# Kernel tuning notes

Hardware: AMD Instinct MI355X
Metric: run time of the kernel (lower is better)

The kernel has to match this reference:

```python
import jax, jax.numpy as jnp
import numpy as np

# --- config (matches init_kwargs) ---
H = 16          # num_attention_heads
DH = 64         # size_per_head
U = H * DH      # units = 1024
M = 8           # num_memory_slots
L = M + 1       # memory slots + current input row
R = 2 * M + 1   # relative position range
EPS = 1e-6
FORGET_BIAS = 1.0
INPUT_BIAS = 0.0
SCALE = 1.0 / np.sqrt(DH)


def _rel_emb():
    # sinusoidal relative-position embedding table [2M+1, U]
    p = np.arange(-M, M + 1, dtype=np.float64)
    i = np.arange(U)
    expo = np.where(i % 2 == 0, i, i - 1) / U
    ang = p[:, None] / np.power(10000.0, expo)[None, :]
    tab = np.where(i % 2 == 0, np.sin(ang), np.cos(ang))
    return jnp.asarray(tab, dtype=jnp.float32)

REL_EMB = _rel_emb()
# rel index table: idx[q,k] = q - k + M  (replaces one-hot pos_table matmul)
_qi = jnp.arange(L)
REL_IDX = _qi[:, None] - _qi[None, :] + M  # [L, L]


def _hard_sigmoid(x):
    return jnp.clip(0.2 * x + 0.5, 0.0, 1.0)


def _ln(x, g, b):
    m = jnp.mean(x, axis=-1, keepdims=True)
    v = jnp.var(x, axis=-1, keepdims=True)
    return (x - m) * jax.lax.rsqrt(v + EPS) * g + b


def setup_inputs() -> dict:
    key = jax.random.key(0)
    ks = jax.random.split(key, 12)
    B, T, DIN = 32, 128, 1024
    s = 0.02
    return {
        "x": jax.random.normal(ks[0], (B, T, DIN), jnp.float32),
        "input_kernel": jax.random.normal(ks[1], (DIN, U), jnp.float32) * s,
        "input_bias": jnp.zeros((U,), jnp.float32),
        "gate_kernel": jax.random.normal(ks[2], (DIN, 2 * U), jnp.float32) * s,
        "recurrent_kernel": jax.random.normal(ks[3], (U, 2 * U), jnp.float32) * s,
        "recurrent_bias": jnp.zeros((2 * U,), jnp.float32),
        "attention_kernel": jax.random.normal(ks[4], (U, 3 * U), jnp.float32) * s,
        "attention_bias": jnp.zeros((3 * U,), jnp.float32),
        "mlp_kernel": jax.random.normal(ks[5], (U, 2 * U), jnp.float32) * s,
        "mlp_bias": jnp.zeros((2 * U,), jnp.float32),
        "ln_gamma": jnp.ones((2 * U,), jnp.float32),
        "ln_beta": jnp.zeros((2 * U,), jnp.float32),
        "rel_kernel": jax.random.normal(ks[6], (U, U), jnp.float32) * s,
    }


def _forward(x, input_kernel, input_bias, gate_kernel, recurrent_kernel,
             recurrent_bias, attention_kernel, attention_bias, mlp_kernel,
             mlp_bias, ln_gamma, ln_beta, rel_kernel):
    B = x.shape[0]
    # relative key projection, shared across steps: [R, H, DH]
    r = (REL_EMB @ rel_kernel).reshape(R, H, DH)

    def step(mem, xt):
        # xt: [B, DIN]; mem: [B, M, U]
        xp = xt @ input_kernel + input_bias              # [B, U]
        mp = jnp.concatenate([mem, xp[:, None, :]], axis=1)  # [B, L, U]
        qkv = mp @ attention_kernel + attention_bias     # [B, L, 3U]
        q, k, v = jnp.split(qkv, 3, axis=-1)
        q = q.reshape(B, L, H, DH).transpose(0, 2, 1, 3)  # [B,H,L,DH]
        k = k.reshape(B, L, H, DH).transpose(0, 2, 1, 3)
        v = v.reshape(B, L, H, DH).transpose(0, 2, 1, 3)
        scores = jnp.einsum('bhqd,bhkd->bhqk', q, k) * SCALE
        rsc = jnp.einsum('bhqd,rhd->bhqr', q, r) * SCALE  # [B,H,L,R]
        scores = scores + rsc[:, :, jnp.arange(L)[:, None], REL_IDX]
        p = jax.nn.softmax(scores, axis=-1)
        attn = jnp.einsum('bhqk,bhkd->bhqd', p, v)
        attn = attn.transpose(0, 2, 1, 3).reshape(B, L, U)
        a1 = _ln(mp + attn, ln_gamma[:U], ln_beta[:U])
        h = jax.nn.gelu(a1 @ mlp_kernel[:, :U] + mlp_bias[:U])
        m2 = h @ mlp_kernel[:, U:] + mlp_bias[U:]
        cand = _ln(a1 + m2, ln_gamma[U:], ln_beta[U:])
        # LSTM-style per-slot gating
        g = (xt @ gate_kernel)[:, None, :] + mp @ recurrent_kernel + recurrent_bias
        ig, fg = jnp.split(g, 2, axis=-1)
        ig = _hard_sigmoid(ig + INPUT_BIAS)
        fg = _hard_sigmoid(fg + FORGET_BIAS)
        nmp = fg * mp + ig * jnp.tanh(cand)              # [B, L, U]
        return nmp[:, :M, :], nmp[:, -1, :]

    mem0 = jnp.zeros((B, M, U), x.dtype)
    _, ys = jax.lax.scan(step, mem0, x.transpose(1, 0, 2))
    return ys.transpose(1, 0, 2)  # [B, T, U]


def reference(x, input_kernel, input_bias, gate_kernel, recurrent_kernel,
              recurrent_bias, attention_kernel, attention_bias, mlp_kernel,
              mlp_bias, ln_gamma, ln_beta, rel_kernel):
    return _forward(x, input_kernel, input_bias, gate_kernel, recurrent_kernel,
                    recurrent_bias, attention_kernel, attention_bias,
                    mlp_kernel, mlp_bias, ln_gamma, ln_beta, rel_kernel)
```

## Files before the change

### kernel.cpp

```cpp
#include <hip/hip_runtime.h>
#include <hip/hip_bf16.h>
#include <math.h>

#define BB 32
#define TT 128
#define UU 1024
#define MM 8
#define LL 9
#define RR 17
#define MROWS 288
#define NKS 4
#define KLEN 256

typedef __bf16 bf16x8 __attribute__((ext_vector_type(8)));
typedef float f32x4 __attribute__((ext_vector_type(4)));
typedef float f32x8 __attribute__((ext_vector_type(8)));

__device__ __forceinline__ void split3(float v, __bf16* x1, __bf16* x2, __bf16* x3)
{
    __bf16 h1 = (__bf16)v;  float r = v - (float)h1;
    __bf16 h2 = (__bf16)r;  r -= (float)h2;
    *x1 = h1; *x2 = h2; *x3 = (__bf16)r;
}

__device__ __forceinline__ void split8(const f32x8 v, bf16x8& a, bf16x8& b, bf16x8& c)
{
#pragma unroll
    for (int j = 0; j < 8; ++j) {
        float f = v[j];
        __bf16 h1 = (__bf16)f; float r = f - (float)h1;
        __bf16 h2 = (__bf16)r; r -= (float)h2;
        a[j] = h1; b[j] = h2; c[j] = (__bf16)r;
    }
}

__device__ __forceinline__ float gelu_f(float x)
{
    float t = tanhf(0.7978845608028654f * (x + 0.044715f * x * x * x));
    return 0.5f * x * (1.f + t);
}

template<int CG>
__global__ __launch_bounds__(256) void gemmks(
    const float* __restrict__ A,
    const __bf16* __restrict__ B1, const __bf16* __restrict__ B2,
    const __bf16* __restrict__ B3,
    float* __restrict__ P, int N, int GdivP)
{
    int tid = threadIdx.x, wave = tid >> 6, lane = tid & 63;
    int bid = blockIdx.x;
    int x = bid & 7, inner = bid >> 3;
    int q = inner % GdivP, rowT = inner / GdivP;
    int g = x + 8 * q;
    int colT = g / NKS, ks = g % NKS;

    int lr = lane & 15, kg = lane >> 4;
    int row0 = rowT * 32 + (wave & 1) * 16;
    int col0 = colT * (CG * 32) + (wave >> 1) * (CG * 16);
    int kbase = ks * KLEN;

    const float* Ap = A + (size_t)(row0 + lr) * 1024 + kbase + kg * 8;
    size_t boff = (size_t)(col0 + lr) * 1024 + kbase + kg * 8;

    f32x4 acc[CG];
#pragma unroll
    for (int c = 0; c < CG; ++c) acc[c] = (f32x4){0.f, 0.f, 0.f, 0.f};

#pragma unroll
    for (int k = 0; k < KLEN; k += 32) {
        f32x8 af = *(const f32x8*)(Ap + k);
        bf16x8 a1, a2, a3;
        split8(af, a1, a2, a3);
#pragma unroll
        for (int c = 0; c < CG; ++c) {
            size_t o = boff + (size_t)c * 16 * 1024 + k;
            bf16x8 b1 = *(const bf16x8*)(B1 + o);
            bf16x8 b2 = *(const bf16x8*)(B2 + o);
            bf16x8 b3 = *(const bf16x8*)(B3 + o);
            acc[c] = __builtin_amdgcn_mfma_f32_16x16x32_bf16(a1, b1, acc[c], 0, 0, 0);
            acc[c] = __builtin_amdgcn_mfma_f32_16x16x32_bf16(a1, b2, acc[c], 0, 0, 0);
            acc[c] = __builtin_amdgcn_mfma_f32_16x16x32_bf16(a2, b1, acc[c], 0, 0, 0);
            acc[c] = __builtin_amdgcn_mfma_f32_16x16x32_bf16(a1, b3, acc[c], 0, 0, 0);
            acc[c] = __builtin_amdgcn_mfma_f32_16x16x32_bf16(a2, b2, acc[c], 0, 0, 0);
            acc[c] = __builtin_amdgcn_mfma_f32_16x16x32_bf16(a3, b1, acc[c], 0, 0, 0);
        }
    }

    int r0 = row0 + kg * 4;
    float* Pk = P + (size_t)ks * MROWS * N;
#pragma unroll
    for (int c = 0; c < CG; ++c) {
        int col = col0 + c * 16 + lr;
#pragma unroll
        for (int r = 0; r < 4; ++r)
            Pk[(size_t)(r0 + r) * N + col] = acc[c][r];
    }
}

__global__ __launch_bounds__(256) void add4(
    const float* __restrict__ P, const float* __restrict__ bias,
    float* __restrict__ out, int N, int act, int total4)
{
    int idx = blockIdx.x * 256 + threadIdx.x;
    if (idx >= total4) return;
    size_t e = (size_t)idx * 4;
    size_t SP = (size_t)MROWS * N;
    int col = (int)(e % N);
    f32x4 p0 = *(const f32x4*)(P + e);
    f32x4 p1 = *(const f32x4*)(P + SP + e);
    f32x4 p2 = *(const f32x4*)(P + 2 * SP + e);
    f32x4 p3 = *(const f32x4*)(P + 3 * SP + e);
    f32x4 bv = *(const f32x4*)(bias + col);
    f32x4 s;
#pragma unroll
    for (int j = 0; j < 4; ++j) {
        float v = ((p0[j] + p1[j]) + (p2[j] + p3[j])) + bv[j];
        s[j] = act ? gelu_f(v) : v;
    }
    *(f32x4*)(out + e) = s;
}

template<int CG>
__device__ __forceinline__ void tile6(
    const float* __restrict__ A,
    const __bf16* __restrict__ B1, const __bf16* __restrict__ B2,
    const __bf16* __restrict__ B3,
    const float* __restrict__ bias, float* __restrict__ C,
    int ldc, int act, int row0, int col0, int lane)
{
    int lr = lane & 15, kofs = (lane >> 4) * 8;
    const float* Ap = A + (size_t)(row0 + lr) * 1024 + kofs;
    size_t boff = (size_t)(col0 + lr) * 1024 + kofs;
    f32x4 acc[CG];
#pragma unroll
    for (int c = 0; c < CG; ++c) acc[c] = (f32x4){0.f, 0.f, 0.f, 0.f};

    for (int k = 0; k < 1024; k += 32) {
        f32x8 af = *(const f32x8*)(Ap + k);
        bf16x8 a1, a2, a3;
        split8(af, a1, a2, a3);
#pragma unroll
        for (int c = 0; c < CG; ++c) {
            size_t o = boff + (size_t)c * 16 * 1024 + k;
            bf16x8 b1 = *(const bf16x8*)(B1 + o);
            bf16x8 b2 = *(const bf16x8*)(B2 + o);
            bf16x8 b3 = *(const bf16x8*)(B3 + o);
            acc[c] = __builtin_amdgcn_mfma_f32_16x16x32_bf16(a1, b1, acc[c], 0, 0, 0);
            acc[c] = __builtin_amdgcn_mfma_f32_16x16x32_bf16(a1, b2, acc[c], 0, 0, 0);
            acc[c] = __builtin_amdgcn_mfma_f32_16x16x32_bf16(a2, b1, acc[c], 0, 0, 0);
            acc[c] = __builtin_amdgcn_mfma_f32_16x16x32_bf16(a1, b3, acc[c], 0, 0, 0);
            acc[c] = __builtin_amdgcn_mfma_f32_16x16x32_bf16(a2, b2, acc[c], 0, 0, 0);
            acc[c] = __builtin_amdgcn_mfma_f32_16x16x32_bf16(a3, b1, acc[c], 0, 0, 0);
        }
    }

    int r0 = row0 + (lane >> 4) * 4;
#pragma unroll
    for (int c = 0; c < CG; ++c) {
        int col = col0 + c * 16 + lr;
        float bv = bias ? bias[col] : 0.f;
#pragma unroll
        for (int r = 0; r < 4; ++r) {
            float v = acc[c][r] + bv;
            if (act == 1) v = gelu_f(v);
            C[(size_t)(r0 + r) * ldc + col] = v;
        }
    }
}

__global__ __launch_bounds__(256) void gemm6(
    const float* __restrict__ A,
    const __bf16* __restrict__ B1, const __bf16* __restrict__ B2,
    const __bf16* __restrict__ B3,
    const float* __restrict__ bias, float* __restrict__ C, int ldc, int act)
{
    int wave = threadIdx.x >> 6, lane = threadIdx.x & 63;
    int row0 = blockIdx.y * 32 + (wave >> 1) * 16;
    int col0 = blockIdx.x * 128 + (wave & 1) * 64;
    tile6<4>(A, B1, B2, B3, bias, C, ldc, act, row0, col0, lane);
}

__global__ __launch_bounds__(256) void transpose_split(
    const float* __restrict__ in,
    __bf16* __restrict__ o1, __bf16* __restrict__ o2, __bf16* __restrict__ o3,
    int N)
{
    __shared__ float t[32][33];
    int tx = threadIdx.x & 31, ty = threadIdx.x >> 5;
    int k0 = blockIdx.y * 32, n0 = blockIdx.x * 32;
#pragma unroll
    for (int i = 0; i < 4; ++i)
        t[ty + i * 8][tx] = in[(size_t)(k0 + ty + i * 8) * N + n0 + tx];
    __syncthreads();
#pragma unroll
    for (int i = 0; i < 4; ++i) {
        float v = t[tx][ty + i * 8];
        size_t off = (size_t)(n0 + ty + i * 8) * 1024 + k0 + tx;
        split3(v, o1 + off, o2 + off, o3 + off);
    }
}

#define BKK 16
__global__ __launch_bounds__(256) void gemm_f32(
    const float* __restrict__ A, const float* __restrict__ B,
    float* __restrict__ C, int M, int N, int K)
{
    __shared__ float As[BKK][65];
    __shared__ float Bs[BKK][64];
    int tid = threadIdx.x;
    int row0 = blockIdx.y * 64, col0 = blockIdx.x * 64;
    int ty = tid >> 4, tx = tid & 15;
    float acc[4][4];
#pragma unroll
    for (int i = 0; i < 4; ++i)
#pragma unroll
        for (int j = 0; j < 4; ++j) acc[i][j] = 0.f;
    for (int k0 = 0; k0 < K; k0 += BKK) {
        {
            int r = tid >> 2, kv = (tid & 3) * 4;
            float4 v = make_float4(0.f, 0.f, 0.f, 0.f);
            int gr = row0 + r;
            if (gr < M) v = *(const float4*)(A + (size_t)gr * K + k0 + kv);
            As[kv + 0][r] = v.x; As[kv + 1][r] = v.y;
            As[kv + 2][r] = v.z; As[kv + 3][r] = v.w;
        }
        {
            int r = tid >> 4, cv = (tid & 15) * 4;
            float4 v = *(const float4*)(B + (size_t)(k0 + r) * N + col0 + cv);
            *(float4*)&Bs[r][cv] = v;
        }
        __syncthreads();
#pragma unroll
        for (int kk = 0; kk < BKK; ++kk) {
            float a[4], b[4];
#pragma unroll
            for (int j = 0; j < 4; ++j) a[j] = As[kk][ty * 4 + j];
#pragma unroll
            for (int j = 0; j < 4; ++j) b[j] = Bs[kk][tx * 4 + j];
#pragma unroll
            for (int i = 0; i < 4; ++i)
#pragma unroll
                for (int j = 0; j < 4; ++j) acc[i][j] += a[i] * b[j];
        }
        __syncthreads();
    }
#pragma unroll
    for (int i = 0; i < 4; ++i) {
        int gr = row0 + ty * 4 + i;
        if (gr >= M) continue;
#pragma unroll
        for (int j = 0; j < 4; ++j)
            C[(size_t)gr * N + col0 + tx * 4 + j] = acc[i][j];
    }
}

__global__ void relemb_kernel(float* __restrict__ tab)
{
    int p = blockIdx.x;
    float pv = (float)(p - MM);
    for (int i = threadIdx.x; i < UU; i += blockDim.x) {
        float expo = (float)(i & ~1) * (1.0f / (float)UU);
        float scale = exp2f(-expo * 13.287712379549449f);
        float ang = pv * scale;
        tab[p * UU + i] = (i & 1) ? cosf(ang) : sinf(ang);
    }
}

__global__ void init_mp(const float* __restrict__ xp_all, float* __restrict__ mp)
{
    int row = blockIdx.x;
    int b = row / LL, l = row % LL;
    for (int u = threadIdx.x; u < UU; u += blockDim.x)
        mp[(size_t)row * UU + u] = (l == MM) ? xp_all[((size_t)b * TT) * UU + u] : 0.f;
}

__global__ __launch_bounds__(512) void attn_ln(
    const float* __restrict__ qkvg, const float* __restrict__ rproj,
    const float* __restrict__ mp,
    const float* __restrict__ gamma, const float* __restrict__ beta,
    float* __restrict__ a1)
{
    __shared__ float sA[LL][UU];
    __shared__ float red[16];
    int b = blockIdx.x;
    int tid = threadIdx.x;
    int wave = tid >> 6, lane = tid & 63;

    for (int hh = 0; hh < 2; ++hh) {
        int h = wave + hh * 8;
        const float* base = qkvg + (size_t)b * LL * 5120 + h * 64 + lane;
        float q[LL], k[LL], v[LL], r[RR];
#pragma unroll
        for (int l = 0; l < LL; ++l) {
            q[l] = base[l * 5120];
            k[l] = base[l * 5120 + 1024];
            v[l] = base[l * 5120 + 2048];
        }
#pragma unroll
        for (int rp = 0; rp < RR; ++rp) r[rp] = rproj[rp * UU + h * 64 + lane];
#pragma unroll
        for (int qr = 0; qr < LL; ++qr) {
            float sc[LL];
#pragma unroll
            for (int kr = 0; kr < LL; ++kr) {
                float prod = q[qr] * (k[kr] + r[qr - kr + MM]);
#pragma unroll
                for (int o = 32; o > 0; o >>= 1) prod += __shfl_xor(prod, o);
                sc[kr] = prod * 0.125f;
            }
            float m = sc[0];
#pragma unroll
            for (int kr = 1; kr < LL; ++kr) m = fmaxf(m, sc[kr]);
            float s = 0.f;
#pragma unroll
            for (int kr = 0; kr < LL; ++kr) { sc[kr] = expf(sc[kr] - m); s += sc[kr]; }
            float inv = 1.0f / s;
            float acc = 0.f;
#pragma unroll
            for (int kr = 0; kr < LL; ++kr) acc += sc[kr] * v[kr];
            sA[qr][h * 64 + lane] = acc * inv;
        }
    }
    __syncthreads();

    for (int l = 0; l < LL; ++l) {
        size_t row = (size_t)(b * LL + l);
        float x0 = mp[row * UU + tid] + sA[l][tid];
        float x1 = mp[row * UU + tid + 512] + sA[l][tid + 512];
        float s = x0 + x1, ss = x0 * x0 + x1 * x1;
#pragma unroll
        for (int o = 32; o > 0; o >>= 1) { s += __shfl_xor(s, o); ss += __shfl_xor(ss, o); }
        if (lane == 0) { red[wave * 2] = s; red[wave * 2 + 1] = ss; }
        __syncthreads();
        float S = 0.f, SS = 0.f;
#pragma unroll
        for (int w = 0; w < 8; ++w) { S += red[w * 2]; SS += red[w * 2 + 1]; }
        __syncthreads();
        float mean = S * (1.0f / UU);
        float var = SS * (1.0f / UU) - mean * mean;
        float rstd = rsqrtf(var + 1e-6f);
        a1[row * UU + tid]       = (x0 - mean) * rstd * gamma[tid] + beta[tid];
        a1[row * UU + tid + 512] = (x1 - mean) * rstd * gamma[tid + 512] + beta[tid + 512];
    }
}

__global__ __launch_bounds__(256) void finalize_step(
    const float* __restrict__ a1, const float* __restrict__ m2P,
    const float* __restrict__ bm,
    const float* __restrict__ qkvg, const float* __restrict__ gx_all,
    const float* __restrict__ xp_all,
    const float* __restrict__ gamma, const float* __restrict__ beta,
    float* __restrict__ mp, float* __restrict__ out, int t)
{
    __shared__ float red[8];
    int row = blockIdx.x;
    int b = row / LL, l = row % LL;
    int tid = threadIdx.x;
    int wave = tid >> 6, lane = tid & 63;
    const size_t SP = (size_t)MROWS * UU;

    float x[4];
    float s = 0.f, ss = 0.f;
#pragma unroll
    for (int j = 0; j < 4; ++j) {
        int u = tid + j * 256;
        size_t off = (size_t)row * UU + u;
        float m2v = ((m2P[off] + m2P[SP + off]) + (m2P[2 * SP + off] + m2P[3 * SP + off]))
                    + bm[1024 + u];
        x[j] = a1[off] + m2v;
        s += x[j]; ss += x[j] * x[j];
    }
#pragma unroll
    for (int o = 32; o > 0; o >>= 1) { s += __shfl_xor(s, o); ss += __shfl_xor(ss, o); }
    if (lane == 0) { red[wave * 2] = s; red[wave * 2 + 1] = ss; }
    __syncthreads();
    float S = 0.f, SS = 0.f;
#pragma unroll
    for (int w = 0; w < 4; ++w) { S += red[w * 2]; SS += red[w * 2 + 1]; }
    float mean = S * (1.0f / UU);
    float rstd = rsqrtf(SS * (1.0f / UU) - mean * mean + 1e-6f);

    size_t gxoff = ((size_t)b * TT + t) * 2048;
    size_t grow = (size_t)row * 5120 + 3072;
#pragma unroll
    for (int j = 0; j < 4; ++j) {
        int u = tid + j * 256;
        float cand = (x[j] - mean) * rstd * gamma[1024 + u] + beta[1024 + u];
        float tc = tanhf(cand);
        float gi = gx_all[gxoff + u]        + qkvg[grow + u];
        float gf = gx_all[gxoff + 1024 + u] + qkvg[grow + 1024 + u];
        float ig = fminf(fmaxf(0.2f * gi + 0.5f, 0.f), 1.f);
        float fg = fminf(fmaxf(0.2f * (gf + 1.0f) + 0.5f, 0.f), 1.f);
        size_t off = (size_t)row * UU + u;
        float nmp = fg * mp[off] + ig * tc;
        if (l < MM) {
            mp[off] = nmp;
        } else {
            out[((size_t)b * TT + t) * UU + u] = nmp;
            if (t + 1 < TT)
                mp[off] = xp_all[((size_t)b * TT + t + 1) * UU + u];
        }
    }
}

extern "C" void kernel_launch(void* const* d_in, const int* in_sizes, int n_in,
                              void* d_out, int out_size, void* d_ws, size_t ws_size,
                              hipStream_t stream)
{
    const float* x    = (const float*)d_in[0];
    const float* Wi   = (const float*)d_in[1];
    const float* bi   = (const float*)d_in[2];
    const float* Wg   = (const float*)d_in[3];
    const float* Wr   = (const float*)d_in[4];
    const float* br   = (const float*)d_in[5];
    const float* Wa   = (const float*)d_in[6];
    const float* ba   = (const float*)d_in[7];
    const float* Wm   = (const float*)d_in[8];
    const float* bm   = (const float*)d_in[9];
    const float* gam  = (const float*)d_in[10];
    const float* bet  = (const float*)d_in[11];
    const float* Wrel = (const float*)d_in[12];
    float* out = (float*)d_out;

    char* w = (char*)d_ws;
    float*  xp_all = (float*)w;  w += (size_t)BB*TT*UU*4;
    float*  gx_all = (float*)w;  w += (size_t)BB*TT*2048*4;
    size_t W1N = (size_t)5120 * 1024, WMN = (size_t)2048 * 1024;
    __bf16* W1a = (__bf16*)w;    w += W1N*2;
    __bf16* W1b = (__bf16*)w;    w += W1N*2;
    __bf16* W1c = (__bf16*)w;    w += W1N*2;
    __bf16* Wma = (__bf16*)w;    w += WMN*2;
    __bf16* Wmb = (__bf16*)w;    w += WMN*2;
    __bf16* Wmc = (__bf16*)w;    w += WMN*2;
    float*  b1    = (float*)w;   w += 5120*4;
    float*  tab   = (float*)w;   w += RR*UU*4;
    float*  rproj = (float*)w;   w += RR*UU*4;
    float*  mp    = (float*)w;   w += (size_t)MROWS*UU*4;
    float*  qkvg  = (float*)w;   w += (size_t)MROWS*5120*4;
    float*  a1    = (float*)w;   w += (size_t)MROWS*UU*4;
    float*  hbuf  = (float*)w;   w += (size_t)MROWS*UU*4;
    char* sbase = w;
    float*  qkvgP = (float*)w;   w += (size_t)NKS*MROWS*5120*4;
    float*  m1P   = (float*)w;   w += (size_t)NKS*MROWS*UU*4;
    float*  m2P   = (float*)w;   w += (size_t)NKS*MROWS*UU*4;
    __bf16* Wia = (__bf16*)sbase;
    __bf16* Wib = Wia + (size_t)1024 * 1024;
    __bf16* Wic = Wib + (size_t)1024 * 1024;
    __bf16* Wga = Wic + (size_t)1024 * 1024;
    __bf16* Wgb = Wga + (size_t)2048 * 1024;
    __bf16* Wgc = Wgb + (size_t)2048 * 1024;

    relemb_kernel<<<RR, 256, 0, stream>>>(tab);
    gemm_f32<<<dim3(UU / 64, 1), 256, 0, stream>>>(tab, Wrel, rproj, RR, UU, UU);
    transpose_split<<<dim3(3072 / 32, 32), 256, 0, stream>>>(Wa, W1a, W1b, W1c, 3072);
    transpose_split<<<dim3(2048 / 32, 32), 256, 0, stream>>>(
        Wr, W1a + (size_t)3072 * 1024, W1b + (size_t)3072 * 1024,
        W1c + (size_t)3072 * 1024, 2048);
    transpose_split<<<dim3(2048 / 32, 32), 256, 0, stream>>>(Wm, Wma, Wmb, Wmc, 2048);
    transpose_split<<<dim3(1024 / 32, 32), 256, 0, stream>>>(Wi, Wia, Wib, Wic, 1024);
    transpose_split<<<dim3(2048 / 32, 32), 256, 0, stream>>>(Wg, Wga, Wgb, Wgc, 2048);
    hipMemcpyAsync(b1, ba, 3072 * sizeof(float), hipMemcpyDeviceToDevice, stream);
    hipMemcpyAsync(b1 + 3072, br, 2048 * sizeof(float), hipMemcpyDeviceToDevice, stream);
    gemm6<<<dim3(UU / 128, (BB * TT) / 32), 256, 0, stream>>>(
        x, Wia, Wib, Wic, bi, xp_all, UU, 0);
    gemm6<<<dim3(2048 / 128, (BB * TT) / 32), 256, 0, stream>>>(
        x, Wga, Wgb, Wgc, nullptr, gx_all, 2048, 0);
    init_mp<<<MROWS, 256, 0, stream>>>(xp_all, mp);

    for (int t = 0; t < TT; ++t) {
        gemmks<2><<<2880, 256, 0, stream>>>(mp, W1a, W1b, W1c, qkvgP, 5120, 40);
        add4<<<(MROWS * 5120 / 4 + 255) / 256, 256, 0, stream>>>(
            qkvgP, b1, qkvg, 5120, 0, MROWS * 5120 / 4);
        attn_ln<<<BB, 512, 0, stream>>>(qkvg, rproj, mp, gam, bet, a1);
        gemmks<2><<<576, 256, 0, stream>>>(a1, Wma, Wmb, Wmc, m1P, UU, 8);
        add4<<<(MROWS * UU / 4 + 255) / 256, 256, 0, stream>>>(
            m1P, bm, hbuf, UU, 1, MROWS * UU / 4);
        gemmks<2><<<576, 256, 0, stream>>>(hbuf, Wma + (size_t)1024 * 1024,
                                           Wmb + (size_t)1024 * 1024,
                                           Wmc + (size_t)1024 * 1024, m2P, UU, 8);
        finalize_step<<<MROWS, 256, 0, stream>>>(a1, m2P, bm, qkvg, gx_all, xp_all,
                                                 gam, bet, mp, out, t);
    }
}
```

Baseline: 25.07 ms.

## Fold QKVG split-K reduction into consumers and prefetch B fragments in gemmks

The big per-step QKVG GEMM now uses 2 K-splits of 512 instead of 4 of 256, which halves the partial-sum traffic. The separate add4 reduction kernel is removed, and attn_ln and finalize_step sum the two partials plus bias directly. The gemmks inner loop also loads B fragments for two K-chunks ahead of the MFMAs to overlap loads with compute. In exchange there are fewer blocks for the QKVG GEMM (1440 instead of 2880), and each consumer does extra reads of the partial buffers.

```diff
diff --git a/kernel.cpp b/kernel.cpp
--- a/kernel.cpp
+++ b/kernel.cpp
@@ -9,8 +9,6 @@
 #define LL 9
 #define RR 17
 #define MROWS 288
-#define NKS 4
-#define KLEN 256
 
 typedef __bf16 bf16x8 __attribute__((ext_vector_type(8)));
 typedef float f32x4 __attribute__((ext_vector_type(4)));
@@ -40,7 +38,7 @@
     return 0.5f * x * (1.f + t);
 }
 
-template<int CG>
+template<int CG, int NKS, int KLEN>
 __global__ __launch_bounds__(256) void gemmks(
     const float* __restrict__ A,
     const __bf16* __restrict__ B1, const __bf16* __restrict__ B2,
@@ -66,8 +64,84 @@
 #pragma unroll
     for (int c = 0; c < CG; ++c) acc[c] = (f32x4){0.f, 0.f, 0.f, 0.f};
 
-#pragma unroll
-    for (int k = 0; k < KLEN; k += 32) {
+    for (int kc = 0; kc < KLEN; kc += 64) {
+        f32x8 af0 = *(const f32x8*)(Ap + kc);
+        f32x8 af1 = *(const f32x8*)(Ap + kc + 32);
+        bf16x8 bv[2][CG][3];
+#pragma unroll
+        for (int h = 0; h < 2; ++h)
+#pragma unroll
+            for (int c = 0; c < CG; ++c) {
+                size_t o = boff + (size_t)c * 16 * 1024 + kc + h * 32;
+                bv[h][c][0] = *(const bf16x8*)(B1 + o);
+                bv[h][c][1] = *(const bf16x8*)(B2 + o);
+                bv[h][c][2] = *(const bf16x8*)(B3 + o);
+            }
+#pragma unroll
+        for (int h = 0; h < 2; ++h) {
+            bf16x8 a1, a2, a3;
+            split8(h ? af1 : af0, a1, a2, a3);
+#pragma unroll
+            for (int c = 0; c < CG; ++c) {
+                bf16x8 b1 = bv[h][c][0], b2 = bv[h][c][1], b3 = bv[h][c][2];
+                acc[c] = __builtin_amdgcn_mfma_f32_16x16x32_bf16(a1, b1, acc[c], 0, 0, 0);
+                acc[c] = __builtin_amdgcn_mfma_f32_16x16x32_bf16(a1, b2, acc[c], 0, 0, 0);
+                acc[c] = __builtin_amdgcn_mfma_f32_16x16x32_bf16(a2, b1, acc[c], 0, 0, 0);
+                acc[c] = __builtin_amdgcn_mfma_f32_16x16x32_bf16(a1, b3, acc[c], 0, 0, 0);
+                acc[c] = __builtin_amdgcn_mfma_f32_16x16x32_bf16(a2, b2, acc[c], 0, 0, 0);
+                acc[c] = __builtin_amdgcn_mfma_f32_16x16x32_bf16(a3, b1, acc[c], 0, 0, 0);
+            }
+        }
+    }
+
+    int r0 = row0 + kg * 4;
+    float* Pk = P + (size_t)ks * MROWS * N;
+#pragma unroll
+    for (int c = 0; c < CG; ++c) {
+        int col = col0 + c * 16 + lr;
+#pragma unroll
+        for (int r = 0; r < 4; ++r)
+            Pk[(size_t)(r0 + r) * N + col] = acc[c][r];
+    }
+}
+
+__global__ __launch_bounds__(256) void add4gelu(
+    const float* __restrict__ P, const float* __restrict__ bias,
+    float* __restrict__ out, int N, int total4)
+{
+    int idx = blockIdx.x * 256 + threadIdx.x;
+    if (idx >= total4) return;
+    size_t e = (size_t)idx * 4;
+    size_t SP = (size_t)MROWS * N;
+    int col = (int)(e % N);
+    f32x4 p0 = *(const f32x4*)(P + e);
+    f32x4 p1 = *(const f32x4*)(P + SP + e);
+    f32x4 p2 = *(const f32x4*)(P + 2 * SP + e);
+    f32x4 p3 = *(const f32x4*)(P + 3 * SP + e);
+    f32x4 bv = *(const f32x4*)(bias + col);
+    f32x4 s;
+#pragma unroll
+    for (int j = 0; j < 4; ++j)
+        s[j] = gelu_f(((p0[j] + p1[j]) + (p2[j] + p3[j])) + bv[j]);
+    *(f32x4*)(out + e) = s;
+}
+
+template<int CG>
+__device__ __forceinline__ void tile6(
+    const float* __restrict__ A,
+    const __bf16* __restrict__ B1, const __bf16* __restrict__ B2,
+    const __bf16* __restrict__ B3,
+    const float* __restrict__ bias, float* __restrict__ C,
+    int ldc, int act, int row0, int col0, int lane)
+{
+    int lr = lane & 15, kofs = (lane >> 4) * 8;
+    const float* Ap = A + (size_t)(row0 + lr) * 1024 + kofs;
+    size_t boff = (size_t)(col0 + lr) * 1024 + kofs;
+    f32x4 acc[CG];
+#pragma unroll
+    for (int c = 0; c < CG; ++c) acc[c] = (f32x4){0.f, 0.f, 0.f, 0.f};
+
+    for (int k = 0; k < 1024; k += 32) {
         f32x8 af = *(const f32x8*)(Ap + k);
         bf16x8 a1, a2, a3;
         split8(af, a1, a2, a3);
@@ -86,74 +160,6 @@
         }
     }
 
-    int r0 = row0 + kg * 4;
-    float* Pk = P + (size_t)ks * MROWS * N;
-#pragma unroll
-    for (int c = 0; c < CG; ++c) {
-        int col = col0 + c * 16 + lr;
-#pragma unroll
-        for (int r = 0; r < 4; ++r)
-            Pk[(size_t)(r0 + r) * N + col] = acc[c][r];
-    }
-}
-
-__global__ __launch_bounds__(256) void add4(
-    const float* __restrict__ P, const float* __restrict__ bias,
-    float* __restrict__ out, int N, int act, int total4)
-{
-    int idx = blockIdx.x * 256 + threadIdx.x;
-    if (idx >= total4) return;
-    size_t e = (size_t)idx * 4;
-    size_t SP = (size_t)MROWS * N;
-    int col = (int)(e % N);
-    f32x4 p0 = *(const f32x4*)(P + e);
-    f32x4 p1 = *(const f32x4*)(P + SP + e);
-    f32x4 p2 = *(const f32x4*)(P + 2 * SP + e);
-    f32x4 p3 = *(const f32x4*)(P + 3 * SP + e);
-    f32x4 bv = *(const f32x4*)(bias + col);
-    f32x4 s;
-#pragma unroll
-    for (int j = 0; j < 4; ++j) {
-        float v = ((p0[j] + p1[j]) + (p2[j] + p3[j])) + bv[j];
-        s[j] = act ? gelu_f(v) : v;
-    }
-    *(f32x4*)(out + e) = s;
-}
-
-template<int CG>
-__device__ __forceinline__ void tile6(
-    const float* __restrict__ A,
-    const __bf16* __restrict__ B1, const __bf16* __restrict__ B2,
-    const __bf16* __restrict__ B3,
-    const float* __restrict__ bias, float* __restrict__ C,
-    int ldc, int act, int row0, int col0, int lane)
-{
-    int lr = lane & 15, kofs = (lane >> 4) * 8;
-    const float* Ap = A + (size_t)(row0 + lr) * 1024 + kofs;
-    size_t boff = (size_t)(col0 + lr) * 1024 + kofs;
-    f32x4 acc[CG];
-#pragma unroll
-    for (int c = 0; c < CG; ++c) acc[c] = (f32x4){0.f, 0.f, 0.f, 0.f};
-
-    for (int k = 0; k < 1024; k += 32) {
-        f32x8 af = *(const f32x8*)(Ap + k);
-        bf16x8 a1, a2, a3;
-        split8(af, a1, a2, a3);
-#pragma unroll
-        for (int c = 0; c < CG; ++c) {
-            size_t o = boff + (size_t)c * 16 * 1024 + k;
-            bf16x8 b1 = *(const bf16x8*)(B1 + o);
-            bf16x8 b2 = *(const bf16x8*)(B2 + o);
-            bf16x8 b3 = *(const bf16x8*)(B3 + o);
-            acc[c] = __builtin_amdgcn_mfma_f32_16x16x32_bf16(a1, b1, acc[c], 0, 0, 0);
-            acc[c] = __builtin_amdgcn_mfma_f32_16x16x32_bf16(a1, b2, acc[c], 0, 0, 0);
-            acc[c] = __builtin_amdgcn_mfma_f32_16x16x32_bf16(a2, b1, acc[c], 0, 0, 0);
-            acc[c] = __builtin_amdgcn_mfma_f32_16x16x32_bf16(a1, b3, acc[c], 0, 0, 0);
-            acc[c] = __builtin_amdgcn_mfma_f32_16x16x32_bf16(a2, b2, acc[c], 0, 0, 0);
-            acc[c] = __builtin_amdgcn_mfma_f32_16x16x32_bf16(a3, b1, acc[c], 0, 0, 0);
-        }
-    }
-
     int r0 = row0 + (lane >> 4) * 4;
 #pragma unroll
     for (int c = 0; c < CG; ++c) {
@@ -275,7 +281,8 @@
 }
 
 __global__ __launch_bounds__(512) void attn_ln(
-    const float* __restrict__ qkvg, const float* __restrict__ rproj,
+    const float* __restrict__ qkvgP, const float* __restrict__ b1,
+    const float* __restrict__ rproj,
     const float* __restrict__ mp,
     const float* __restrict__ gamma, const float* __restrict__ beta,
     float* __restrict__ a1)
@@ -285,19 +292,23 @@
     int b = blockIdx.x;
     int tid = threadIdx.x;
     int wave = tid >> 6, lane = tid & 63;
+    const size_t SPA = (size_t)MROWS * 5120;
 
     for (int hh = 0; hh < 2; ++hh) {
         int h = wave + hh * 8;
-        const float* base = qkvg + (size_t)b * LL * 5120 + h * 64 + lane;
+        int cq = h * 64 + lane;
+        const float* base0 = qkvgP + (size_t)b * LL * 5120 + cq;
+        const float* base1 = base0 + SPA;
+        float bq = b1[cq], bk = b1[1024 + cq], bvv = b1[2048 + cq];
         float q[LL], k[LL], v[LL], r[RR];
 #pragma unroll
         for (int l = 0; l < LL; ++l) {
-            q[l] = base[l * 5120];
-            k[l] = base[l * 5120 + 1024];
-            v[l] = base[l * 5120 + 2048];
-        }
-#pragma unroll
-        for (int rp = 0; rp < RR; ++rp) r[rp] = rproj[rp * UU + h * 64 + lane];
+            q[l] = (base0[l * 5120]        + base1[l * 5120])        + bq;
+            k[l] = (base0[l * 5120 + 1024] + base1[l * 5120 + 1024]) + bk;
+            v[l] = (base0[l * 5120 + 2048] + base1[l * 5120 + 2048]) + bvv;
+        }
+#pragma unroll
+        for (int rp = 0; rp < RR; ++rp) r[rp] = rproj[rp * UU + cq];
 #pragma unroll
         for (int qr = 0; qr < LL; ++qr) {
             float sc[LL];
@@ -347,7 +358,8 @@
 __global__ __launch_bounds__(256) void finalize_step(
     const float* __restrict__ a1, const float* __restrict__ m2P,
     const float* __restrict__ bm,
-    const float* __restrict__ qkvg, const float* __restrict__ gx_all,
+    const float* __restrict__ qkvgP, const float* __restrict__ b1,
+    const float* __restrict__ gx_all,
     const float* __restrict__ xp_all,
     const float* __restrict__ gamma, const float* __restrict__ beta,
     float* __restrict__ mp, float* __restrict__ out, int t)
@@ -358,6 +370,7 @@
     int tid = threadIdx.x;
     int wave = tid >> 6, lane = tid & 63;
     const size_t SP = (size_t)MROWS * UU;
+    const size_t SPA = (size_t)MROWS * 5120;
 
     float x[4];
     float s = 0.f, ss = 0.f;
@@ -387,8 +400,10 @@
         int u = tid + j * 256;
         float cand = (x[j] - mean) * rstd * gamma[1024 + u] + beta[1024 + u];
         float tc = tanhf(cand);
-        float gi = gx_all[gxoff + u]        + qkvg[grow + u];
-        float gf = gx_all[gxoff + 1024 + u] + qkvg[grow + 1024 + u];
+        float gri = (qkvgP[grow + u]        + qkvgP[SPA + grow + u])        + b1[3072 + u];
+        float grf = (qkvgP[grow + 1024 + u] + qkvgP[SPA + grow + 1024 + u]) + b1[4096 + u];
+        float gi = gx_all[gxoff + u]        + gri;
+        float gf = gx_all[gxoff + 1024 + u] + grf;
         float ig = fminf(fmaxf(0.2f * gi + 0.5f, 0.f), 1.f);
         float fg = fminf(fmaxf(0.2f * (gf + 1.0f) + 0.5f, 0.f), 1.f);
         size_t off = (size_t)row * UU + u;
@@ -436,13 +451,12 @@
     float*  tab   = (float*)w;   w += RR*UU*4;
     float*  rproj = (float*)w;   w += RR*UU*4;
     float*  mp    = (float*)w;   w += (size_t)MROWS*UU*4;
-    float*  qkvg  = (float*)w;   w += (size_t)MROWS*5120*4;
     float*  a1    = (float*)w;   w += (size_t)MROWS*UU*4;
     float*  hbuf  = (float*)w;   w += (size_t)MROWS*UU*4;
     char* sbase = w;
-    float*  qkvgP = (float*)w;   w += (size_t)NKS*MROWS*5120*4;
-    float*  m1P   = (float*)w;   w += (size_t)NKS*MROWS*UU*4;
-    float*  m2P   = (float*)w;   w += (size_t)NKS*MROWS*UU*4;
+    float*  qkvgP = (float*)w;   w += (size_t)2*MROWS*5120*4;
+    float*  m1P   = (float*)w;   w += (size_t)4*MROWS*UU*4;
+    float*  m2P   = (float*)w;   w += (size_t)4*MROWS*UU*4;
     __bf16* Wia = (__bf16*)sbase;
     __bf16* Wib = Wia + (size_t)1024 * 1024;
     __bf16* Wic = Wib + (size_t)1024 * 1024;
@@ -468,17 +482,15 @@
     init_mp<<<MROWS, 256, 0, stream>>>(xp_all, mp);
 
     for (int t = 0; t < TT; ++t) {
-        gemmks<2><<<2880, 256, 0, stream>>>(mp, W1a, W1b, W1c, qkvgP, 5120, 40);
-        add4<<<(MROWS * 5120 / 4 + 255) / 256, 256, 0, stream>>>(
-            qkvgP, b1, qkvg, 5120, 0, MROWS * 5120 / 4);
-        attn_ln<<<BB, 512, 0, stream>>>(qkvg, rproj, mp, gam, bet, a1);
-        gemmks<2><<<576, 256, 0, stream>>>(a1, Wma, Wmb, Wmc, m1P, UU, 8);
-        add4<<<(MROWS * UU / 4 + 255) / 256, 256, 0, stream>>>(
-            m1P, bm, hbuf, UU, 1, MROWS * UU / 4);
-        gemmks<2><<<576, 256, 0, stream>>>(hbuf, Wma + (size_t)1024 * 1024,
-                                           Wmb + (size_t)1024 * 1024,
-                                           Wmc + (size_t)1024 * 1024, m2P, UU, 8);
-        finalize_step<<<MROWS, 256, 0, stream>>>(a1, m2P, bm, qkvg, gx_all, xp_all,
-                                                 gam, bet, mp, out, t);
-    }
-}
+        gemmks<2, 2, 512><<<1440, 256, 0, stream>>>(mp, W1a, W1b, W1c,
+                                                    qkvgP, 5120, 20);
+        attn_ln<<<BB, 512, 0, stream>>>(qkvgP, b1, rproj, mp, gam, bet, a1);
+        gemmks<2, 4, 256><<<576, 256, 0, stream>>>(a1, Wma, Wmb, Wmc, m1P, UU, 8);
+        add4gelu<<<MROWS, 256, 0, stream>>>(m1P, bm, hbuf, UU, MROWS * UU / 4);
+        gemmks<2, 4, 256><<<576, 256, 0, stream>>>(hbuf, Wma + (size_t)1024 * 1024,
+                                                   Wmb + (size_t)1024 * 1024,
+                                                   Wmc + (size_t)1024 * 1024, m2P, UU, 8);
+        finalize_step<<<MROWS, 256, 0, stream>>>(a1, m2P, bm, qkvgP, b1, gx_all,
+                                                 xp_all, gam, bet, mp, out, t);
+    }
+}
```

After: 26.39 ms. 5.2% more time.

## Replace 3-way bf16 split GEMMs with scaled 2-way fp16 split

Applied to the files above, without the earlier changes.

Switches the fp32-emulating matrix products from a three-term bf16 decomposition (six MFMAs per tile) to a two-term fp16 decomposition with a residual scaled by 4096 (three MFMAs, split into main and residual accumulators). This halves the matrix-core work and cuts weight bytes read per step from three copies to two. The gemmks loop is also restructured to preload weight fragments for two k-chunks before issuing MFMAs. The fp16 range and the residual scaling could lose accuracy or underflow for small values, and precision against the fp32 reference may shift.

```diff
diff --git a/kernel.cpp b/kernel.cpp
--- a/kernel.cpp
+++ b/kernel.cpp
@@ -9,28 +9,28 @@
 #define LL 9
 #define RR 17
 #define MROWS 288
-#define NKS 4
-#define KLEN 256
-
-typedef __bf16 bf16x8 __attribute__((ext_vector_type(8)));
+#define RSC 4096.0f
+#define RSCI (1.0f/4096.0f)
+
+typedef _Float16 f16x8 __attribute__((ext_vector_type(8)));
 typedef float f32x4 __attribute__((ext_vector_type(4)));
 typedef float f32x8 __attribute__((ext_vector_type(8)));
 
-__device__ __forceinline__ void split3(float v, __bf16* x1, __bf16* x2, __bf16* x3)
-{
-    __bf16 h1 = (__bf16)v;  float r = v - (float)h1;
-    __bf16 h2 = (__bf16)r;  r -= (float)h2;
-    *x1 = h1; *x2 = h2; *x3 = (__bf16)r;
-}
-
-__device__ __forceinline__ void split8(const f32x8 v, bf16x8& a, bf16x8& b, bf16x8& c)
+__device__ __forceinline__ void split2(float v, _Float16* h1, _Float16* h2)
+{
+    _Float16 a = (_Float16)v;
+    float r = (v - (float)a) * RSC;
+    *h1 = a; *h2 = (_Float16)r;
+}
+
+__device__ __forceinline__ void split2x8(const f32x8 v, f16x8& a, f16x8& b)
 {
 #pragma unroll
     for (int j = 0; j < 8; ++j) {
         float f = v[j];
-        __bf16 h1 = (__bf16)f; float r = f - (float)h1;
-        __bf16 h2 = (__bf16)r; r -= (float)h2;
-        a[j] = h1; b[j] = h2; c[j] = (__bf16)r;
+        _Float16 h1 = (_Float16)f;
+        float r = (f - (float)h1) * RSC;
+        a[j] = h1; b[j] = (_Float16)r;
     }
 }
 
@@ -40,11 +40,10 @@
     return 0.5f * x * (1.f + t);
 }
 
-template<int CG>
+template<int CG, int NKS, int KLEN>
 __global__ __launch_bounds__(256) void gemmks(
     const float* __restrict__ A,
-    const __bf16* __restrict__ B1, const __bf16* __restrict__ B2,
-    const __bf16* __restrict__ B3,
+    const _Float16* __restrict__ B1, const _Float16* __restrict__ B2,
     float* __restrict__ P, int N, int GdivP)
 {
     int tid = threadIdx.x, wave = tid >> 6, lane = tid & 63;
@@ -62,27 +61,35 @@
     const float* Ap = A + (size_t)(row0 + lr) * 1024 + kbase + kg * 8;
     size_t boff = (size_t)(col0 + lr) * 1024 + kbase + kg * 8;
 
-    f32x4 acc[CG];
-#pragma unroll
-    for (int c = 0; c < CG; ++c) acc[c] = (f32x4){0.f, 0.f, 0.f, 0.f};
-
-#pragma unroll
-    for (int k = 0; k < KLEN; k += 32) {
-        f32x8 af = *(const f32x8*)(Ap + k);
-        bf16x8 a1, a2, a3;
-        split8(af, a1, a2, a3);
-#pragma unroll
-        for (int c = 0; c < CG; ++c) {
-            size_t o = boff + (size_t)c * 16 * 1024 + k;
-            bf16x8 b1 = *(const bf16x8*)(B1 + o);
-            bf16x8 b2 = *(const bf16x8*)(B2 + o);
-            bf16x8 b3 = *(const bf16x8*)(B3 + o);
-            acc[c] = __builtin_amdgcn_mfma_f32_16x16x32_bf16(a1, b1, acc[c], 0, 0, 0);
-            acc[c] = __builtin_amdgcn_mfma_f32_16x16x32_bf16(a1, b2, acc[c], 0, 0, 0);
-            acc[c] = __builtin_amdgcn_mfma_f32_16x16x32_bf16(a2, b1, acc[c], 0, 0, 0);
-            acc[c] = __builtin_amdgcn_mfma_f32_16x16x32_bf16(a1, b3, acc[c], 0, 0, 0);
-            acc[c] = __builtin_amdgcn_mfma_f32_16x16x32_bf16(a2, b2, acc[c], 0, 0, 0);
-            acc[c] = __builtin_amdgcn_mfma_f32_16x16x32_bf16(a3, b1, acc[c], 0, 0, 0);
+    f32x4 accM[CG], accR[CG];
+#pragma unroll
+    for (int c = 0; c < CG; ++c) {
+        accM[c] = (f32x4){0.f, 0.f, 0.f, 0.f};
+        accR[c] = (f32x4){0.f, 0.f, 0.f, 0.f};
+    }
+
+    for (int kc = 0; kc < KLEN; kc += 64) {
+        f32x8 af0 = *(const f32x8*)(Ap + kc);
+        f32x8 af1 = *(const f32x8*)(Ap + kc + 32);
+        f16x8 bv[2][CG][2];
+#pragma unroll
+        for (int h = 0; h < 2; ++h)
+#pragma unroll
+            for (int c = 0; c < CG; ++c) {
+                size_t o = boff + (size_t)c * 16 * 1024 + kc + h * 32;
+                bv[h][c][0] = *(const f16x8*)(B1 + o);
+                bv[h][c][1] = *(const f16x8*)(B2 + o);
+            }
+#pragma unroll
+        for (int h = 0; h < 2; ++h) {
+            f16x8 a1, a2s;
+            split2x8(h ? af1 : af0, a1, a2s);
+#pragma unroll
+            for (int c = 0; c < CG; ++c) {
+                accM[c] = __builtin_amdgcn_mfma_f32_16x16x32_f16(a1, bv[h][c][0], accM[c], 0, 0, 0);
+                accR[c] = __builtin_amdgcn_mfma_f32_16x16x32_f16(a1, bv[h][c][1], accR[c], 0, 0, 0);
+                accR[c] = __builtin_amdgcn_mfma_f32_16x16x32_f16(a2s, bv[h][c][0], accR[c], 0, 0, 0);
+            }
         }
     }
 
@@ -93,7 +100,7 @@
         int col = col0 + c * 16 + lr;
 #pragma unroll
         for (int r = 0; r < 4; ++r)
-            Pk[(size_t)(r0 + r) * N + col] = acc[c][r];
+            Pk[(size_t)(r0 + r) * N + col] = accM[c][r] + accR[c][r] * RSCI;
     }
 }
 
@@ -120,70 +127,54 @@
     *(f32x4*)(out + e) = s;
 }
 
-template<int CG>
-__device__ __forceinline__ void tile6(
+__global__ __launch_bounds__(256) void gemm2(
     const float* __restrict__ A,
-    const __bf16* __restrict__ B1, const __bf16* __restrict__ B2,
-    const __bf16* __restrict__ B3,
-    const float* __restrict__ bias, float* __restrict__ C,
-    int ldc, int act, int row0, int col0, int lane)
-{
+    const _Float16* __restrict__ B1, const _Float16* __restrict__ B2,
+    const float* __restrict__ bias, float* __restrict__ C, int ldc, int act)
+{
+    int wave = threadIdx.x >> 6, lane = threadIdx.x & 63;
+    int row0 = blockIdx.y * 32 + (wave >> 1) * 16;
+    int col0 = blockIdx.x * 128 + (wave & 1) * 64;
     int lr = lane & 15, kofs = (lane >> 4) * 8;
     const float* Ap = A + (size_t)(row0 + lr) * 1024 + kofs;
     size_t boff = (size_t)(col0 + lr) * 1024 + kofs;
-    f32x4 acc[CG];
-#pragma unroll
-    for (int c = 0; c < CG; ++c) acc[c] = (f32x4){0.f, 0.f, 0.f, 0.f};
-
+    f32x4 accM[4], accR[4];
+#pragma unroll
+    for (int c = 0; c < 4; ++c) {
+        accM[c] = (f32x4){0.f, 0.f, 0.f, 0.f};
+        accR[c] = (f32x4){0.f, 0.f, 0.f, 0.f};
+    }
     for (int k = 0; k < 1024; k += 32) {
         f32x8 af = *(const f32x8*)(Ap + k);
-        bf16x8 a1, a2, a3;
-        split8(af, a1, a2, a3);
-#pragma unroll
-        for (int c = 0; c < CG; ++c) {
+        f16x8 a1, a2s;
+        split2x8(af, a1, a2s);
+#pragma unroll
+        for (int c = 0; c < 4; ++c) {
             size_t o = boff + (size_t)c * 16 * 1024 + k;
-            bf16x8 b1 = *(const bf16x8*)(B1 + o);
-            bf16x8 b2 = *(const bf16x8*)(B2 + o);
-            bf16x8 b3 = *(const bf16x8*)(B3 + o);
-            acc[c] = __builtin_amdgcn_mfma_f32_16x16x32_bf16(a1, b1, acc[c], 0, 0, 0);
-            acc[c] = __builtin_amdgcn_mfma_f32_16x16x32_bf16(a1, b2, acc[c], 0, 0, 0);
-            acc[c] = __builtin_amdgcn_mfma_f32_16x16x32_bf16(a2, b1, acc[c], 0, 0, 0);
-            acc[c] = __builtin_amdgcn_mfma_f32_16x16x32_bf16(a1, b3, acc[c], 0, 0, 0);
-            acc[c] = __builtin_amdgcn_mfma_f32_16x16x32_bf16(a2, b2, acc[c], 0, 0, 0);
-            acc[c] = __builtin_amdgcn_mfma_f32_16x16x32_bf16(a3, b1, acc[c], 0, 0, 0);
-        }
-    }
-
+            f16x8 b1 = *(const f16x8*)(B1 + o);
+            f16x8 b2 = *(const f16x8*)(B2 + o);
+            accM[c] = __builtin_amdgcn_mfma_f32_16x16x32_f16(a1, b1, accM[c], 0, 0, 0);
+            accR[c] = __builtin_amdgcn_mfma_f32_16x16x32_f16(a1, b2, accR[c], 0, 0, 0);
+            accR[c] = __builtin_amdgcn_mfma_f32_16x16x32_f16(a2s, b1, accR[c], 0, 0, 0);
+        }
+    }
     int r0 = row0 + (lane >> 4) * 4;
 #pragma unroll
-    for (int c = 0; c < CG; ++c) {
+    for (int c = 0; c < 4; ++c) {
         int col = col0 + c * 16 + lr;
         float bv = bias ? bias[col] : 0.f;
 #pragma unroll
         for (int r = 0; r < 4; ++r) {
-            float v = acc[c][r] + bv;
+            float v = accM[c][r] + accR[c][r] * RSCI + bv;
             if (act == 1) v = gelu_f(v);
             C[(size_t)(r0 + r) * ldc + col] = v;
         }
     }
 }
 
-__global__ __launch_bounds__(256) void gemm6(
-    const float* __restrict__ A,
-    const __bf16* __restrict__ B1, const __bf16* __restrict__ B2,
-    const __bf16* __restrict__ B3,
-    const float* __restrict__ bias, float* __restrict__ C, int ldc, int act)
-{
-    int wave = threadIdx.x >> 6, lane = threadIdx.x & 63;
-    int row0 = blockIdx.y * 32 + (wave >> 1) * 16;
-    int col0 = blockIdx.x * 128 + (wave & 1) * 64;
-    tile6<4>(A, B1, B2, B3, bias, C, ldc, act, row0, col0, lane);
-}
-
 __global__ __launch_bounds__(256) void transpose_split(
     const float* __restrict__ in,
-    __bf16* __restrict__ o1, __bf16* __restrict__ o2, __bf16* __restrict__ o3,
-    int N)
+    _Float16* __restrict__ o1, _Float16* __restrict__ o2, int N)
 {
     __shared__ float t[32][33];
     int tx = threadIdx.x & 31, ty = threadIdx.x >> 5;
@@ -196,7 +187,7 @@
     for (int i = 0; i < 4; ++i) {
         float v = t[tx][ty + i * 8];
         size_t off = (size_t)(n0 + ty + i * 8) * 1024 + k0 + tx;
-        split3(v, o1 + off, o2 + off, o3 + off);
+        split2(v, o1 + off, o2 + off);
     }
 }
 
@@ -426,12 +417,10 @@
     float*  xp_all = (float*)w;  w += (size_t)BB*TT*UU*4;
     float*  gx_all = (float*)w;  w += (size_t)BB*TT*2048*4;
     size_t W1N = (size_t)5120 * 1024, WMN = (size_t)2048 * 1024;
-    __bf16* W1a = (__bf16*)w;    w += W1N*2;
-    __bf16* W1b = (__bf16*)w;    w += W1N*2;
-    __bf16* W1c = (__bf16*)w;    w += W1N*2;
-    __bf16* Wma = (__bf16*)w;    w += WMN*2;
-    __bf16* Wmb = (__bf16*)w;    w += WMN*2;
-    __bf16* Wmc = (__bf16*)w;    w += WMN*2;
+    _Float16* W1a = (_Float16*)w;  w += W1N*2;
+    _Float16* W1b = (_Float16*)w;  w += W1N*2;
+    _Float16* Wma = (_Float16*)w;  w += WMN*2;
+    _Float16* Wmb = (_Float16*)w;  w += WMN*2;
     float*  b1    = (float*)w;   w += 5120*4;
     float*  tab   = (float*)w;   w += RR*UU*4;
     float*  rproj = (float*)w;   w += RR*UU*4;
@@ -440,44 +429,40 @@
     float*  a1    = (float*)w;   w += (size_t)MROWS*UU*4;
     float*  hbuf  = (float*)w;   w += (size_t)MROWS*UU*4;
     char* sbase = w;
-    float*  qkvgP = (float*)w;   w += (size_t)NKS*MROWS*5120*4;
-    float*  m1P   = (float*)w;   w += (size_t)NKS*MROWS*UU*4;
-    float*  m2P   = (float*)w;   w += (size_t)NKS*MROWS*UU*4;
-    __bf16* Wia = (__bf16*)sbase;
-    __bf16* Wib = Wia + (size_t)1024 * 1024;
-    __bf16* Wic = Wib + (size_t)1024 * 1024;
-    __bf16* Wga = Wic + (size_t)1024 * 1024;
-    __bf16* Wgb = Wga + (size_t)2048 * 1024;
-    __bf16* Wgc = Wgb + (size_t)2048 * 1024;
+    float*  qkvgP = (float*)w;   w += (size_t)4*MROWS*5120*4;
+    float*  m1P   = (float*)w;   w += (size_t)4*MROWS*UU*4;
+    float*  m2P   = (float*)w;   w += (size_t)4*MROWS*UU*4;
+    _Float16* Wia = (_Float16*)sbase;
+    _Float16* Wib = Wia + (size_t)1024 * 1024;
+    _Float16* Wga = Wib + (size_t)1024 * 1024;
+    _Float16* Wgb = Wga + (size_t)2048 * 1024;
 
     relemb_kernel<<<RR, 256, 0, stream>>>(tab);
     gemm_f32<<<dim3(UU / 64, 1), 256, 0, stream>>>(tab, Wrel, rproj, RR, UU, UU);
-    transpose_split<<<dim3(3072 / 32, 32), 256, 0, stream>>>(Wa, W1a, W1b, W1c, 3072);
+    transpose_split<<<dim3(3072 / 32, 32), 256, 0, stream>>>(Wa, W1a, W1b, 3072);
     transpose_split<<<dim3(2048 / 32, 32), 256, 0, stream>>>(
-        Wr, W1a + (size_t)3072 * 1024, W1b + (size_t)3072 * 1024,
-        W1c + (size_t)3072 * 1024, 2048);
-    transpose_split<<<dim3(2048 / 32, 32), 256, 0, stream>>>(Wm, Wma, Wmb, Wmc, 2048);
-    transpose_split<<<dim3(1024 / 32, 32), 256, 0, stream>>>(Wi, Wia, Wib, Wic, 1024);
-    transpose_split<<<dim3(2048 / 32, 32), 256, 0, stream>>>(Wg, Wga, Wgb, Wgc, 2048);
+        Wr, W1a + (size_t)3072 * 1024, W1b + (size_t)3072 * 1024, 2048);
+    transpose_split<<<dim3(2048 / 32, 32), 256, 0, stream>>>(Wm, Wma, Wmb, 2048);
+    transpose_split<<<dim3(1024 / 32, 32), 256, 0, stream>>>(Wi, Wia, Wib, 1024);
+    transpose_split<<<dim3(2048 / 32, 32), 256, 0, stream>>>(Wg, Wga, Wgb, 2048);
     hipMemcpyAsync(b1, ba, 3072 * sizeof(float), hipMemcpyDeviceToDevice, stream);
     hipMemcpyAsync(b1 + 3072, br, 2048 * sizeof(float), hipMemcpyDeviceToDevice, stream);
-    gemm6<<<dim3(UU / 128, (BB * TT) / 32), 256, 0, stream>>>(
-        x, Wia, Wib, Wic, bi, xp_all, UU, 0);
-    gemm6<<<dim3(2048 / 128, (BB * TT) / 32), 256, 0, stream>>>(
-        x, Wga, Wgb, Wgc, nullptr, gx_all, 2048, 0);
+    gemm2<<<dim3(UU / 128, (BB * TT) / 32), 256, 0, stream>>>(
+        x, Wia, Wib, bi, xp_all, UU, 0);
+    gemm2<<<dim3(2048 / 128, (BB * TT) / 32), 256, 0, stream>>>(
+        x, Wga, Wgb, nullptr, gx_all, 2048, 0);
     init_mp<<<MROWS, 256, 0, stream>>>(xp_all, mp);
 
     for (int t = 0; t < TT; ++t) {
-        gemmks<2><<<2880, 256, 0, stream>>>(mp, W1a, W1b, W1c, qkvgP, 5120, 40);
+        gemmks<2, 4, 256><<<2880, 256, 0, stream>>>(mp, W1a, W1b, qkvgP, 5120, 40);
         add4<<<(MROWS * 5120 / 4 + 255) / 256, 256, 0, stream>>>(
             qkvgP, b1, qkvg, 5120, 0, MROWS * 5120 / 4);
         attn_ln<<<BB, 512, 0, stream>>>(qkvg, rproj, mp, gam, bet, a1);
-        gemmks<2><<<576, 256, 0, stream>>>(a1, Wma, Wmb, Wmc, m1P, UU, 8);
+        gemmks<2, 4, 256><<<576, 256, 0, stream>>>(a1, Wma, Wmb, m1P, UU, 8);
         add4<<<(MROWS * UU / 4 + 255) / 256, 256, 0, stream>>>(
             m1P, bm, hbuf, UU, 1, MROWS * UU / 4);
-        gemmks<2><<<576, 256, 0, stream>>>(hbuf, Wma + (size_t)1024 * 1024,
-                                           Wmb + (size_t)1024 * 1024,
-                                           Wmc + (size_t)1024 * 1024, m2P, UU, 8);
+        gemmks<2, 4, 256><<<576, 256, 0, stream>>>(hbuf, Wma + (size_t)1024 * 1024,
+                                                   Wmb + (size_t)1024 * 1024, m2P, UU, 8);
         finalize_step<<<MROWS, 256, 0, stream>>>(a1, m2P, bm, qkvg, gx_all, xp_all,
                                                  gam, bet, mp, out, t);
     }
```

Result: faster. 20.88 ms, median of 2 (-16.7%).
